# Kernel optimization log

Measured on AMD Instinct MI355X. Metric: run time of the kernel, lower is better.

Reference implementation:

```python
import jax, jax.numpy as jnp
import numpy as np

B, S, D = 2, 2048, 1024
H = 16
HD = D // H  # head_dim = 64
EPS = 1e-5


def _layernorm(x, g, b):
    mu = jnp.mean(x, axis=-1, keepdims=True)
    var = jnp.mean(jnp.square(x - mu), axis=-1, keepdims=True)
    return (x - mu) * jax.lax.rsqrt(var + EPS) * g + b


def setup_inputs() -> dict:
    key = jax.random.key(0)
    ks = jax.random.split(key, 6)
    # Xavier-normal-ish init for projection weights (torch Linear layout: [out, in])
    std = float(np.sqrt(2.0 / (D + D)))
    return {
        "query": jax.random.normal(ks[0], (B, S, D), dtype=jnp.float32),
        "q_w": jax.random.normal(ks[1], (D, D), dtype=jnp.float32) * std,
        "q_b": jnp.zeros((D,), jnp.float32),
        "k_w": jax.random.normal(ks[2], (D, D), dtype=jnp.float32) * std,
        "k_b": jnp.zeros((D,), jnp.float32),
        "v_w": jax.random.normal(ks[3], (D, D), dtype=jnp.float32) * std,
        "v_b": jnp.zeros((D,), jnp.float32),
        "o_w": jax.random.normal(ks[4], (D, D), dtype=jnp.float32) * std,
        "o_b": jnp.zeros((D,), jnp.float32),
        "q_ln_g": jnp.ones((HD,), jnp.float32),
        "q_ln_b": jnp.zeros((HD,), jnp.float32),
        "k_ln_g": jnp.ones((HD,), jnp.float32),
        "k_ln_b": jnp.zeros((HD,), jnp.float32),
    }


def reference(query, q_w, q_b, k_w, k_b, v_w, v_b, o_w, o_b,
              q_ln_g, q_ln_b, k_ln_g, k_ln_b) -> jnp.ndarray:
    # Self-attention: key = value = query
    q = query @ q_w.T + q_b           # [B, S, D]
    k = query @ k_w.T + k_b
    v = query @ v_w.T + v_b
    q = q.reshape(B, S, H, HD)
    k = k.reshape(B, S, H, HD)
    v = v.reshape(B, S, H, HD)
    # Per-head QK LayerNorm (ViT-22B stabilization)
    q = _layernorm(q, q_ln_g, q_ln_b)
    k = _layernorm(k, k_ln_g, k_ln_b)
    scale = 1.0 / jnp.sqrt(jnp.asarray(HD, q.dtype))
    attn = jnp.einsum("bqhd,bkhd->bhqk", q, k) * scale  # [B, H, Sq, Skv]
    attn = jax.nn.softmax(attn, axis=-1)
    out = jnp.einsum("bhqk,bkhd->bqhd", attn, v)        # [B, Sq, H, HD]
    out = out.reshape(B, S, D)
    return out @ o_w.T + o_b
```

## Files before the change

### kernel.cpp

```cpp
#include <hip/hip_runtime.h>
#include <hip/hip_bf16.h>

typedef float f32x4 __attribute__((ext_vector_type(4)));
typedef __bf16 bf16x8 __attribute__((ext_vector_type(8)));
typedef unsigned short ushort8 __attribute__((ext_vector_type(8)));
typedef unsigned short ushort4e __attribute__((ext_vector_type(4)));

#define SEQ 2048
#define LOG2E 1.4426950408889634f

__device__ __forceinline__ unsigned short f2bf(float f) {
    unsigned int u = __builtin_bit_cast(unsigned int, f);
    unsigned int r = (u + 0x7FFFu + ((u >> 16) & 1u)) >> 16;
    return (unsigned short)r;
}

__device__ __forceinline__ void gload_lds16(const unsigned short* g, unsigned short* l) {
    __builtin_amdgcn_global_load_lds(
        (const __attribute__((address_space(1))) unsigned int*)g,
        (__attribute__((address_space(3))) unsigned int*)l, 16, 0, 0);
}

__global__ __launch_bounds__(256) void conv_bf16(
    const float* __restrict__ s0, const float* __restrict__ s1,
    const float* __restrict__ s2, const float* __restrict__ s3,
    const float* __restrict__ s4,
    unsigned short* __restrict__ d0, unsigned short* __restrict__ d1,
    unsigned short* __restrict__ d2, unsigned short* __restrict__ d3,
    unsigned short* __restrict__ d4)
{
    const int seg = blockIdx.y;
    const float* s = seg == 0 ? s0 : seg == 1 ? s1 : seg == 2 ? s2 : seg == 3 ? s3 : s4;
    unsigned short* d = seg == 0 ? d0 : seg == 1 ? d1 : seg == 2 ? d2 : seg == 3 ? d3 : d4;
    const int n = seg == 0 ? (4096 * 1024) : (1024 * 1024);
    const int i = (blockIdx.x * 256 + threadIdx.x) * 8;
    if (i >= n) return;
    float4 a = *(const float4*)(s + i);
    float4 b = *(const float4*)(s + i + 4);
    ushort8 o;
    o[0] = f2bf(a.x); o[1] = f2bf(a.y); o[2] = f2bf(a.z); o[3] = f2bf(a.w);
    o[4] = f2bf(b.x); o[5] = f2bf(b.y); o[6] = f2bf(b.z); o[7] = f2bf(b.w);
    *(ushort8*)(d + i) = o;
}

__global__ __launch_bounds__(256) void gemm_bf16(
    const unsigned short* __restrict__ A,
    const unsigned short* __restrict__ W0, const unsigned short* __restrict__ W1,
    const unsigned short* __restrict__ W2,
    const float* __restrict__ b0, const float* __restrict__ b1, const float* __restrict__ b2,
    const float* __restrict__ ln_g0, const float* __restrict__ ln_b0,
    const float* __restrict__ ln_g1, const float* __restrict__ ln_b1,
    unsigned short* __restrict__ qn, unsigned short* __restrict__ kn,
    unsigned short* __restrict__ vt,
    float* __restrict__ Cout, int fixed_mode)
{
    const int z = fixed_mode < 0 ? (int)blockIdx.z : fixed_mode;
    const unsigned short* W = (z == 1) ? W1 : (z == 2) ? W2 : W0;
    const float* bias = (z == 1) ? b1 : (z == 2) ? b2 : b0;

    const int bm = blockIdx.y * 128;
    const int bn = blockIdx.x * 128;

    __shared__ unsigned short As[128 * 64];
    __shared__ unsigned short Bs[128 * 64];

    const int t    = threadIdx.x;
    const int lane = t & 63;
    const int wid  = t >> 6;
    const int l15  = lane & 15;
    const int lhi  = lane >> 4;
    const int wm   = (wid >> 1) * 64;
    const int wn   = (wid & 1) * 64;

    const int schunk = (lane & 7) ^ ((lane >> 3) & 7);
    const unsigned short* Ag = A + (size_t)(bm + (lane >> 3)) * 1024 + schunk * 8;
    const unsigned short* Wg = W + (size_t)(bn + (lane >> 3)) * 1024 + schunk * 8;

    f32x4 acc[4][4];
#pragma unroll
    for (int i = 0; i < 4; ++i)
#pragma unroll
        for (int j = 0; j < 4; ++j) acc[i][j] = (f32x4)0.f;

#pragma unroll 1
    for (int kt = 0; kt < 1024; kt += 64) {
        __syncthreads();
#pragma unroll
        for (int c = 0; c < 4; ++c) {
            const int ch = wid * 4 + c;
            gload_lds16(Ag + (size_t)ch * 8 * 1024 + kt, &As[ch * 512]);
            gload_lds16(Wg + (size_t)ch * 8 * 1024 + kt, &Bs[ch * 512]);
        }
        __syncthreads();
#pragma unroll
        for (int kk = 0; kk < 2; ++kk) {
            const int rchunk = ((kk * 4 + lhi) ^ (l15 & 7)) * 8;
            bf16x8 af[4], bw[4];
#pragma unroll
            for (int mi = 0; mi < 4; ++mi)
                af[mi] = __builtin_bit_cast(bf16x8,
                    *(const ushort8*)(&As[(wm + mi * 16 + l15) * 64 + rchunk]));
#pragma unroll
            for (int ni = 0; ni < 4; ++ni)
                bw[ni] = __builtin_bit_cast(bf16x8,
                    *(const ushort8*)(&Bs[(wn + ni * 16 + l15) * 64 + rchunk]));
#pragma unroll
            for (int mi = 0; mi < 4; ++mi)
#pragma unroll
                for (int ni = 0; ni < 4; ++ni)
                    acc[mi][ni] = __builtin_amdgcn_mfma_f32_16x16x32_bf16(af[mi], bw[ni], acc[mi][ni], 0, 0, 0);
        }
    }
    __syncthreads();

    if (z == 3) {
#pragma unroll
        for (int ni = 0; ni < 4; ++ni) {
            const int col = bn + wn + ni * 16 + l15;
            const float bv = bias[col];
#pragma unroll
            for (int mi = 0; mi < 4; ++mi) {
                const int row = bm + wm + mi * 16 + lhi * 4;
#pragma unroll
                for (int r = 0; r < 4; ++r)
                    Cout[(size_t)(row + r) * 1024 + col] = acc[mi][ni][r] + bv;
            }
        }
        return;
    }

    unsigned short* stg = ((wid & 2) ? Bs : As) + (wid & 1) * 4096;
    const int h = (bn + wn) >> 6;

    if (z == 2) {
        float biasv[4];
#pragma unroll
        for (int ni = 0; ni < 4; ++ni) biasv[ni] = bias[bn + wn + ni * 16 + l15];
#pragma unroll
        for (int mi = 0; mi < 4; ++mi)
#pragma unroll
            for (int ni = 0; ni < 4; ++ni)
#pragma unroll
                for (int r = 0; r < 4; ++r)
                    stg[(ni * 16 + l15) * 64 + 32 * (mi >> 1) + lhi * 8 + 2 * r + (mi & 1)] =
                        f2bf(acc[mi][ni][r] + biasv[ni]);
        __builtin_amdgcn_s_waitcnt(0);
        const int srow0 = bm + wm;
        const int b = srow0 >> 11, sbase = srow0 & 2047;
#pragma unroll
        for (int i = 0; i < 8; ++i) {
            const int dl = i * 8 + (lane >> 3);
            const ushort8 v = *(const ushort8*)(&stg[dl * 64 + (((lane & 7) ^ (dl & 7)) * 8)]);
            *(ushort8*)(&vt[((size_t)((b * 16 + h) * 64 + dl)) * 2048 + sbase + (lane & 7) * 8]) = v;
        }
        return;
    }

    const float* g  = (z == 0) ? ln_g0 : ln_g1;
    const float* bb = (z == 0) ? ln_b0 : ln_b1;
    unsigned short* outp = (z == 0) ? qn : kn;
    const float scale = (z == 0) ? 0.125f * LOG2E : 1.0f;
    const int sxor = (z == 1) ? 7 : 0;
    float gv[4], bbv[4], biasv[4];
#pragma unroll
    for (int ni = 0; ni < 4; ++ni) {
        const int d = ni * 16 + l15;
        gv[ni] = g[d]; bbv[ni] = bb[d]; biasv[ni] = bias[bn + wn + d];
    }
#pragma unroll
    for (int mi = 0; mi < 4; ++mi) {
#pragma unroll
        for (int r = 0; r < 4; ++r) {
            float x0 = acc[mi][0][r] + biasv[0];
            float x1 = acc[mi][1][r] + biasv[1];
            float x2 = acc[mi][2][r] + biasv[2];
            float x3 = acc[mi][3][r] + biasv[3];
            float sum = (x0 + x1) + (x2 + x3);
#pragma unroll
            for (int off = 1; off < 16; off <<= 1) sum += __shfl_xor(sum, off);
            const float mean = sum * (1.f / 64.f);
            const float d0 = x0 - mean, d1 = x1 - mean, d2 = x2 - mean, d3 = x3 - mean;
            float vs = (d0 * d0 + d1 * d1) + (d2 * d2 + d3 * d3);
#pragma unroll
            for (int off = 1; off < 16; off <<= 1) vs += __shfl_xor(vs, off);
            const float rstd = rsqrtf(vs * (1.f / 64.f) + 1e-5f);
            const int rl = mi * 16 + lhi * 4 + r;
            stg[rl * 64 +  0 + l15] = f2bf((d0 * rstd * gv[0] + bbv[0]) * scale);
            stg[rl * 64 + 16 + l15] = f2bf((d1 * rstd * gv[1] + bbv[1]) * scale);
            stg[rl * 64 + 32 + l15] = f2bf((d2 * rstd * gv[2] + bbv[2]) * scale);
            stg[rl * 64 + 48 + l15] = f2bf((d3 * rstd * gv[3] + bbv[3]) * scale);
        }
    }
    __builtin_amdgcn_s_waitcnt(0);
#pragma unroll
    for (int i = 0; i < 8; ++i) {
        const int rl  = i * 8 + (lane >> 3);
        const int srow = bm + wm + rl;
        const int b = srow >> 11, s = srow & 2047;
        const ushort8 v = *(const ushort8*)(&stg[rl * 64 + (((lane & 7) ^ (rl & sxor)) * 8)]);
        *(ushort8*)(&outp[((size_t)((b * 16 + h) * 2048 + s)) * 64 + (lane & 7) * 8]) = v;
    }
}

__global__ __launch_bounds__(512) void attn(
    const unsigned short* __restrict__ qn, const unsigned short* __restrict__ kn,
    const unsigned short* __restrict__ vt, unsigned short* __restrict__ o)
{
    __shared__ unsigned short Ks[3][64 * 64];
    __shared__ unsigned short Vs[3][64 * 64];
    __shared__ unsigned short Ps[128 * 64];

    const int tid  = threadIdx.x;
    const int lane = tid & 63;
    const int w    = tid >> 6;
    const int l15  = lane & 15;
    const int lhi  = lane >> 4;

    const int q0 = blockIdx.x * 128;
    const int bh = blockIdx.y;

    const unsigned short* qrp = qn + ((size_t)bh * SEQ + q0 + w * 16 + l15) * 64 + lhi * 8;
    const bf16x8 aq0 = __builtin_bit_cast(bf16x8, *(const ushort8*)(qrp));
    const bf16x8 aq1 = __builtin_bit_cast(bf16x8, *(const ushort8*)(qrp + 32));

    const unsigned short* kg = kn + ((size_t)bh * SEQ + w * 8 + (lane >> 3)) * 64 + (lane & 7) * 8;
    const unsigned short* vg = vt + ((size_t)bh * 64 + w * 8 + (lane >> 3)) * 2048 + (lane & 7) * 8;

    unsigned short* Kc = &Ks[0][0]; unsigned short* Vc = &Vs[0][0];
    unsigned short* Kn_ = &Ks[1][0]; unsigned short* Vn_ = &Vs[1][0];
    unsigned short* Kf = &Ks[2][0]; unsigned short* Vf = &Vs[2][0];

    f32x4 oacc[4];
#pragma unroll
    for (int nd = 0; nd < 4; ++nd) oacc[nd] = (f32x4)0.f;
    float m_run[4], l_part[4];
#pragma unroll
    for (int i = 0; i < 4; ++i) { m_run[i] = -INFINITY; l_part[i] = 0.f; }

    f32x4 sacc[4];

    auto QK = [&](const unsigned short* kb) {
#pragma unroll
        for (int ni = 0; ni < 4; ++ni) sacc[ni] = (f32x4)0.f;
        __builtin_amdgcn_s_setprio(1);
#pragma unroll
        for (int kk = 0; kk < 2; ++kk) {
            const bf16x8 a = kk ? aq1 : aq0;
#pragma unroll
            for (int ni = 0; ni < 4; ++ni) {
                const int krow = ni * 16 + l15;
                const bf16x8 bk = __builtin_bit_cast(bf16x8,
                    *(const ushort8*)(&kb[krow * 64 + (((kk * 4 + lhi) ^ (krow & 7)) * 8)]));
                sacc[ni] = __builtin_amdgcn_mfma_f32_16x16x32_bf16(a, bk, sacc[ni], 0, 0, 0);
            }
        }
        __builtin_amdgcn_s_setprio(0);
    };

    gload_lds16(kg,                    Kc + w * 512);
    gload_lds16(vg,                    Vc + w * 512);
    gload_lds16(kg + (size_t)64 * 64,  Kn_ + w * 512);
    gload_lds16(vg + 64,               Vn_ + w * 512);
    __builtin_amdgcn_sched_barrier(0);
    asm volatile("s_waitcnt vmcnt(2)" ::: "memory");
    asm volatile("s_barrier" ::: "memory");
    QK(Kc);

#pragma unroll 1
    for (int t = 0; t < 32; ++t) {
        if (t < 30) {
            gload_lds16(kg + (size_t)(t + 2) * 64 * 64, Kf + w * 512);
            gload_lds16(vg + (t + 2) * 64,              Vf + w * 512);
        }
        __builtin_amdgcn_sched_barrier(0);

        float tmax[4];
        float dmax = -1e30f;
#pragma unroll
        for (int r = 0; r < 4; ++r) {
            const float tm = fmaxf(fmaxf(sacc[0][r], sacc[1][r]), fmaxf(sacc[2][r], sacc[3][r]));
            tmax[r] = tm;
            dmax = fmaxf(dmax, tm - m_run[r]);
        }
        if (!__all(dmax <= 8.0f)) {
#pragma unroll
            for (int r = 0; r < 4; ++r) {
                float tm = tmax[r];
#pragma unroll
                for (int off = 1; off < 16; off <<= 1) tm = fmaxf(tm, __shfl_xor(tm, off));
                const float mnew  = fmaxf(m_run[r], tm);
                const float alpha = __builtin_amdgcn_exp2f(m_run[r] - mnew);
                m_run[r] = mnew;
                l_part[r] *= alpha;
#pragma unroll
                for (int nd = 0; nd < 4; ++nd) oacc[nd][r] *= alpha;
            }
        }
#pragma unroll
        for (int r = 0; r < 4; ++r) {
            const float m = m_run[r];
            const float p0 = __builtin_amdgcn_exp2f(sacc[0][r] - m);
            const float p1 = __builtin_amdgcn_exp2f(sacc[1][r] - m);
            const float p2 = __builtin_amdgcn_exp2f(sacc[2][r] - m);
            const float p3 = __builtin_amdgcn_exp2f(sacc[3][r] - m);
            l_part[r] += (p0 + p1) + (p2 + p3);
            unsigned int pk0, pk1;
            asm("v_cvt_pk_bf16_f32 %0, %1, %2" : "=v"(pk0) : "v"(p0), "v"(p1));
            asm("v_cvt_pk_bf16_f32 %0, %1, %2" : "=v"(pk1) : "v"(p2), "v"(p3));
            const int prow = w * 16 + lhi * 4 + r;
            const int rs7  = prow & 7;
            *(unsigned int*)(&Ps[prow * 64 + (((l15 >> 2) ^ rs7) * 8) + 2 * (l15 & 3)]) = pk0;
            *(unsigned int*)(&Ps[prow * 64 + (((4 + (l15 >> 2)) ^ rs7) * 8) + 2 * (l15 & 3)]) = pk1;
        }

        if (t < 31) {
            if (t < 30) { asm volatile("s_waitcnt vmcnt(2)" ::: "memory"); }
            else        { asm volatile("s_waitcnt vmcnt(0)" ::: "memory"); }
            asm volatile("s_barrier" ::: "memory");
            QK(Kn_);
        }

        __builtin_amdgcn_s_setprio(1);
#pragma unroll
        for (int kk = 0; kk < 2; ++kk) {
            const int arow = w * 16 + l15;
            const bf16x8 ap = __builtin_bit_cast(bf16x8,
                *(const ushort8*)(&Ps[arow * 64 + (((kk * 4 + lhi) ^ (arow & 7)) * 8)]));
#pragma unroll
            for (int nd = 0; nd < 4; ++nd) {
                const int vrow = nd * 16 + l15;
                const bf16x8 bv = __builtin_bit_cast(bf16x8,
                    *(const ushort8*)(&Vc[vrow * 64 + (((kk * 4 + lhi) ^ (vrow & 7)) * 8)]));
                oacc[nd] = __builtin_amdgcn_mfma_f32_16x16x32_bf16(ap, bv, oacc[nd], 0, 0, 0);
            }
        }
        __builtin_amdgcn_s_setprio(0);

        if (t < 31) {
            asm volatile("s_barrier" ::: "memory");
        }
        unsigned short* tk = Kc; Kc = Kn_; Kn_ = Kf; Kf = tk;
        unsigned short* tv = Vc; Vc = Vn_; Vn_ = Vf; Vf = tv;
    }

    const int b = bh >> 4, h = bh & 15;
#pragma unroll
    for (int r = 0; r < 4; ++r) {
        float ls = l_part[r];
#pragma unroll
        for (int off = 1; off < 16; off <<= 1) ls += __shfl_xor(ls, off);
        const float inv = 1.f / ls;
        const int qrow = q0 + w * 16 + lhi * 4 + r;
        const size_t base = ((size_t)(b * SEQ + qrow) * 16 + h) * 64;
#pragma unroll
        for (int nd = 0; nd < 4; ++nd)
            o[base + nd * 16 + l15] = f2bf(oacc[nd][r] * inv);
    }
}

extern "C" void kernel_launch(void* const* d_in, const int* in_sizes, int n_in,
                              void* d_out, int out_size, void* d_ws, size_t ws_size,
                              hipStream_t stream)
{
    const float* query  = (const float*)d_in[0];
    const float* q_w    = (const float*)d_in[1];
    const float* q_b    = (const float*)d_in[2];
    const float* k_w    = (const float*)d_in[3];
    const float* k_b    = (const float*)d_in[4];
    const float* v_w    = (const float*)d_in[5];
    const float* v_b    = (const float*)d_in[6];
    const float* o_w    = (const float*)d_in[7];
    const float* o_b    = (const float*)d_in[8];
    const float* q_ln_g = (const float*)d_in[9];
    const float* q_ln_b = (const float*)d_in[10];
    const float* k_ln_g = (const float*)d_in[11];
    const float* k_ln_b = (const float*)d_in[12];

    char* ws = (char*)d_ws;
    unsigned short* qbf = (unsigned short*)(ws);
    unsigned short* wq  = (unsigned short*)(ws + (8ull  << 20));
    unsigned short* wk  = (unsigned short*)(ws + (10ull << 20));
    unsigned short* wv  = (unsigned short*)(ws + (12ull << 20));
    unsigned short* wo  = (unsigned short*)(ws + (14ull << 20));
    unsigned short* qnb = (unsigned short*)(ws + (16ull << 20));
    unsigned short* knb = (unsigned short*)(ws + (24ull << 20));
    unsigned short* vtb = (unsigned short*)(ws + (32ull << 20));
    unsigned short* ofb = (unsigned short*)(ws + (40ull << 20));

    conv_bf16<<<dim3(2048, 5), 256, 0, stream>>>(query, q_w, k_w, v_w, o_w,
                                                 qbf, wq, wk, wv, wo);

    dim3 g1(8, 32, 3);
    gemm_bf16<<<g1, 256, 0, stream>>>(qbf, wq, wk, wv, q_b, k_b, v_b,
                                      q_ln_g, q_ln_b, k_ln_g, k_ln_b,
                                      qnb, knb, vtb, nullptr, -1);

    dim3 g3(16, 32);
    attn<<<g3, 512, 0, stream>>>(qnb, knb, vtb, ofb);

    dim3 g4(8, 32, 1);
    gemm_bf16<<<g4, 256, 0, stream>>>(ofb, wo, wo, wo, o_b, o_b, o_b,
                                      nullptr, nullptr, nullptr, nullptr,
                                      nullptr, nullptr, nullptr, (float*)d_out, 3);
}
```

Measured before the change: 133.7 us.

## Use 4-stage K/V ring buffer, drop trailing barrier, fold max shift into MFMA

```diff
diff --git a/kernel.cpp b/kernel.cpp
--- a/kernel.cpp
+++ b/kernel.cpp
@@ -202,12 +202,12 @@
     }
 }
 
-__global__ __launch_bounds__(512) void attn(
+__global__ __launch_bounds__(512, 4) void attn(
     const unsigned short* __restrict__ qn, const unsigned short* __restrict__ kn,
     const unsigned short* __restrict__ vt, unsigned short* __restrict__ o)
 {
-    __shared__ unsigned short Ks[3][64 * 64];
-    __shared__ unsigned short Vs[3][64 * 64];
+    __shared__ unsigned short Ks[4][64 * 64];
+    __shared__ unsigned short Vs[4][64 * 64];
     __shared__ unsigned short Ps[128 * 64];
 
     const int tid  = threadIdx.x;
@@ -226,83 +226,79 @@
     const unsigned short* kg = kn + ((size_t)bh * SEQ + w * 8 + (lane >> 3)) * 64 + (lane & 7) * 8;
     const unsigned short* vg = vt + ((size_t)bh * 64 + w * 8 + (lane >> 3)) * 2048 + (lane & 7) * 8;
 
-    unsigned short* Kc = &Ks[0][0]; unsigned short* Vc = &Vs[0][0];
-    unsigned short* Kn_ = &Ks[1][0]; unsigned short* Vn_ = &Vs[1][0];
-    unsigned short* Kf = &Ks[2][0]; unsigned short* Vf = &Vs[2][0];
-
     f32x4 oacc[4];
 #pragma unroll
     for (int nd = 0; nd < 4; ++nd) oacc[nd] = (f32x4)0.f;
-    float m_run[4], l_part[4];
-#pragma unroll
-    for (int i = 0; i < 4; ++i) { m_run[i] = -INFINITY; l_part[i] = 0.f; }
+    float l_part[4];
+#pragma unroll
+    for (int i = 0; i < 4; ++i) l_part[i] = 0.f;
+    f32x4 mneg = (f32x4)100.f;
 
     f32x4 sacc[4];
 
     auto QK = [&](const unsigned short* kb) {
-#pragma unroll
-        for (int ni = 0; ni < 4; ++ni) sacc[ni] = (f32x4)0.f;
         __builtin_amdgcn_s_setprio(1);
 #pragma unroll
-        for (int kk = 0; kk < 2; ++kk) {
-            const bf16x8 a = kk ? aq1 : aq0;
-#pragma unroll
-            for (int ni = 0; ni < 4; ++ni) {
-                const int krow = ni * 16 + l15;
-                const bf16x8 bk = __builtin_bit_cast(bf16x8,
-                    *(const ushort8*)(&kb[krow * 64 + (((kk * 4 + lhi) ^ (krow & 7)) * 8)]));
-                sacc[ni] = __builtin_amdgcn_mfma_f32_16x16x32_bf16(a, bk, sacc[ni], 0, 0, 0);
-            }
+        for (int ni = 0; ni < 4; ++ni) {
+            const int krow = ni * 16 + l15;
+            const bf16x8 bk = __builtin_bit_cast(bf16x8,
+                *(const ushort8*)(&kb[krow * 64 + ((lhi ^ (krow & 7)) * 8)]));
+            sacc[ni] = __builtin_amdgcn_mfma_f32_16x16x32_bf16(aq0, bk, mneg, 0, 0, 0);
+        }
+#pragma unroll
+        for (int ni = 0; ni < 4; ++ni) {
+            const int krow = ni * 16 + l15;
+            const bf16x8 bk = __builtin_bit_cast(bf16x8,
+                *(const ushort8*)(&kb[krow * 64 + (((4 + lhi) ^ (krow & 7)) * 8)]));
+            sacc[ni] = __builtin_amdgcn_mfma_f32_16x16x32_bf16(aq1, bk, sacc[ni], 0, 0, 0);
         }
         __builtin_amdgcn_s_setprio(0);
     };
 
-    gload_lds16(kg,                    Kc + w * 512);
-    gload_lds16(vg,                    Vc + w * 512);
-    gload_lds16(kg + (size_t)64 * 64,  Kn_ + w * 512);
-    gload_lds16(vg + 64,               Vn_ + w * 512);
+    gload_lds16(kg,                    &Ks[0][w * 512]);
+    gload_lds16(vg,                    &Vs[0][w * 512]);
+    gload_lds16(kg + (size_t)64 * 64,  &Ks[1][w * 512]);
+    gload_lds16(vg + 64,               &Vs[1][w * 512]);
     __builtin_amdgcn_sched_barrier(0);
     asm volatile("s_waitcnt vmcnt(2)" ::: "memory");
     asm volatile("s_barrier" ::: "memory");
-    QK(Kc);
-
-#pragma unroll 1
+    QK(&Ks[0][0]);
+
+#pragma unroll 4
     for (int t = 0; t < 32; ++t) {
         if (t < 30) {
-            gload_lds16(kg + (size_t)(t + 2) * 64 * 64, Kf + w * 512);
-            gload_lds16(vg + (t + 2) * 64,              Vf + w * 512);
+            gload_lds16(kg + (size_t)(t + 2) * 64 * 64, &Ks[(t + 2) & 3][w * 512]);
+            gload_lds16(vg + (t + 2) * 64,              &Vs[(t + 2) & 3][w * 512]);
         }
         __builtin_amdgcn_sched_barrier(0);
 
         float tmax[4];
-        float dmax = -1e30f;
-#pragma unroll
-        for (int r = 0; r < 4; ++r) {
-            const float tm = fmaxf(fmaxf(sacc[0][r], sacc[1][r]), fmaxf(sacc[2][r], sacc[3][r]));
-            tmax[r] = tm;
-            dmax = fmaxf(dmax, tm - m_run[r]);
-        }
+#pragma unroll
+        for (int r = 0; r < 4; ++r)
+            tmax[r] = fmaxf(fmaxf(sacc[0][r], sacc[1][r]), fmaxf(sacc[2][r], sacc[3][r]));
+        const float dmax = fmaxf(fmaxf(tmax[0], tmax[1]), fmaxf(tmax[2], tmax[3]));
         if (!__all(dmax <= 8.0f)) {
 #pragma unroll
             for (int r = 0; r < 4; ++r) {
                 float tm = tmax[r];
 #pragma unroll
                 for (int off = 1; off < 16; off <<= 1) tm = fmaxf(tm, __shfl_xor(tm, off));
-                const float mnew  = fmaxf(m_run[r], tm);
-                const float alpha = __builtin_amdgcn_exp2f(m_run[r] - mnew);
-                m_run[r] = mnew;
+                const float delta = fmaxf(tm, 0.f);
+                const float alpha = __builtin_amdgcn_exp2f(-delta);
+                mneg[r] -= delta;
                 l_part[r] *= alpha;
 #pragma unroll
                 for (int nd = 0; nd < 4; ++nd) oacc[nd][r] *= alpha;
+#pragma unroll
+                for (int ni = 0; ni < 4; ++ni) sacc[ni][r] -= delta;
             }
         }
 #pragma unroll
         for (int r = 0; r < 4; ++r) {
-            const float m = m_run[r];
-            const float p0 = __builtin_amdgcn_exp2f(sacc[0][r] - m);
-            const float p1 = __builtin_amdgcn_exp2f(sacc[1][r] - m);
-            const float p2 = __builtin_amdgcn_exp2f(sacc[2][r] - m);
-            const float p3 = __builtin_amdgcn_exp2f(sacc[3][r] - m);
+            const float p0 = __builtin_amdgcn_exp2f(sacc[0][r]);
+            const float p1 = __builtin_amdgcn_exp2f(sacc[1][r]);
+            const float p2 = __builtin_amdgcn_exp2f(sacc[2][r]);
+            const float p3 = __builtin_amdgcn_exp2f(sacc[3][r]);
             l_part[r] += (p0 + p1) + (p2 + p3);
             unsigned int pk0, pk1;
             asm("v_cvt_pk_bf16_f32 %0, %1, %2" : "=v"(pk0) : "v"(p0), "v"(p1));
@@ -317,7 +313,7 @@
             if (t < 30) { asm volatile("s_waitcnt vmcnt(2)" ::: "memory"); }
             else        { asm volatile("s_waitcnt vmcnt(0)" ::: "memory"); }
             asm volatile("s_barrier" ::: "memory");
-            QK(Kn_);
+            QK(&Ks[(t + 1) & 3][0]);
         }
 
         __builtin_amdgcn_s_setprio(1);
@@ -330,17 +326,11 @@
             for (int nd = 0; nd < 4; ++nd) {
                 const int vrow = nd * 16 + l15;
                 const bf16x8 bv = __builtin_bit_cast(bf16x8,
-                    *(const ushort8*)(&Vc[vrow * 64 + (((kk * 4 + lhi) ^ (vrow & 7)) * 8)]));
+                    *(const ushort8*)(&Vs[t & 3][vrow * 64 + (((kk * 4 + lhi) ^ (vrow & 7)) * 8)]));
                 oacc[nd] = __builtin_amdgcn_mfma_f32_16x16x32_bf16(ap, bv, oacc[nd], 0, 0, 0);
             }
         }
         __builtin_amdgcn_s_setprio(0);
-
-        if (t < 31) {
-            asm volatile("s_barrier" ::: "memory");
-        }
-        unsigned short* tk = Kc; Kc = Kn_; Kn_ = Kf; Kf = tk;
-        unsigned short* tv = Vc; Vc = Vn_; Vn_ = Vf; Vf = tv;
     }
 
     const int b = bh >> 4, h = bh & 15;
```

After: 130.8 us. 2.2% less time.
